# Kernel optimization log

Measured on AMD Instinct MI355X. Metric: run time of the kernel, lower is better.

The kernel has to match this reference:

```python
import jax, jax.numpy as jnp
import numpy as np

B, L, D_MODEL, N_HEADS = 2, 2048, 1024, 16
D_K = D_MODEL // N_HEADS  # 64
THETA = 10000.0


def setup_inputs() -> dict:
    key = jax.random.key(0)
    k1, k2, k3 = jax.random.split(key, 3)
    std_qkv = (2.0 / (D_MODEL + 3 * D_MODEL)) ** 0.5
    std_out = (2.0 / (D_MODEL + D_MODEL)) ** 0.5
    X = jax.random.normal(k1, (B, L, D_MODEL), dtype=jnp.float32)
    Wqkv = jax.random.truncated_normal(k2, -3.0, 3.0, (3 * D_MODEL, D_MODEL), dtype=jnp.float32) * std_qkv
    Wout = jax.random.truncated_normal(k3, -3.0, 3.0, (D_MODEL, D_MODEL), dtype=jnp.float32) * std_out
    token_positions = jnp.arange(B * L, dtype=jnp.int64 if jax.config.jax_enable_x64 else jnp.int32).reshape(B, L)
    return {"X": X, "token_positions": token_positions, "Wqkv": Wqkv, "Wout": Wout}


def _rope(X, pos):
    # X: (b, h, l, d_k); pos: (b, l)
    k = jnp.arange(D_K // 2, dtype=jnp.float32)
    inv_freq = 1.0 / (THETA ** (2.0 * k / D_K))          # (d_k/2,)
    ang = pos[..., None].astype(jnp.float32) * inv_freq  # (b, l, d_k/2)
    cos = jnp.repeat(jnp.cos(ang), 2, axis=-1)[:, None, :, :].astype(X.dtype)  # (b,1,l,d_k)
    sin = jnp.repeat(jnp.sin(ang), 2, axis=-1)[:, None, :, :].astype(X.dtype)
    # interleaved rotation: (x0,x1,x2,x3,...) -> (-x1,x0,-x3,x2,...)
    X_rot = jnp.stack([-X[..., 1::2], X[..., ::2]], axis=-1).reshape(X.shape)
    return X * cos + X_rot * sin


def reference(X, token_positions, Wqkv, Wout):
    b, l, _ = X.shape
    qkv = jnp.einsum('bld,ed->ble', X, Wqkv)  # (b, l, 3*d_model)
    Q, K, V = jnp.split(qkv, 3, axis=-1)
    to_heads = lambda t: t.reshape(b, l, N_HEADS, D_K).transpose(0, 2, 1, 3)  # (b,h,l,dk)
    Q, K, V = to_heads(Q), to_heads(K), to_heads(V)
    Q = _rope(Q, token_positions)
    K = _rope(K, token_positions)
    scores = jnp.einsum('bhqd,bhkd->bhqk', Q, K) / np.float32(np.sqrt(D_K))
    causal = jnp.tril(jnp.ones((l, l), dtype=bool))  # (l, l)
    scores = jnp.where(causal[None, None], scores.astype(jnp.float32), -jnp.inf)
    weights = jax.nn.softmax(scores, axis=-1).astype(X.dtype)
    out = jnp.einsum('bhqk,bhkd->bhqd', weights, V)
    out = out.transpose(0, 2, 1, 3).reshape(b, l, D_MODEL)
    return jnp.einsum('bld,od->blo', out, Wout)
```

## Files before the change

kernel.cpp:

```cpp
#include <hip/hip_runtime.h>
#include <stdint.h>
#include <stddef.h>
#include <math.h>

#define DEVINL __device__ __forceinline__

typedef __attribute__((ext_vector_type(8))) __bf16 bf16x8;
typedef __attribute__((ext_vector_type(4))) float f32x4;
typedef __attribute__((ext_vector_type(4))) unsigned short us4;
typedef __attribute__((ext_vector_type(8))) unsigned short us8;
typedef __attribute__((ext_vector_type(4))) short short4v;

typedef __attribute__((address_space(1))) unsigned int as1_uint;
typedef __attribute__((address_space(3))) unsigned int as3_uint;

constexpr int SEQ    = 2048;
constexpr int DMODEL = 1024;
constexpr int MTOT   = 4096;
constexpr int NQKV   = 3072;
constexpr int DKH    = 64;

constexpr size_t OFF_XBF  = 0;
constexpr size_t OFF_WQKV = OFF_XBF  + (size_t)MTOT * DMODEL * 2;
constexpr size_t OFF_WOUT = OFF_WQKV + (size_t)NQKV * DMODEL * 2;
constexpr size_t OFF_Q    = OFF_WOUT + (size_t)DMODEL * DMODEL * 2;
constexpr size_t OFF_K    = OFF_Q    + (size_t)MTOT * DMODEL * 2;
constexpr size_t OFF_VT   = OFF_K    + (size_t)MTOT * DMODEL * 2;
constexpr size_t OFF_O    = OFF_VT   + (size_t)MTOT * DMODEL * 2;
constexpr size_t OFF_ROPE = OFF_O    + (size_t)MTOT * DMODEL * 2;

constexpr float QSCALE = 0.125f * 1.4426950408889634f;

DEVINL unsigned short f2bf(float f) {
  unsigned int u = __float_as_uint(f);
  u += 0x7fffu + ((u >> 16) & 1u);
  return (unsigned short)(u >> 16);
}

DEVINL float fexp2(float x) { return __builtin_amdgcn_exp2f(x); }

DEVINL void gld_lds16(const unsigned short* g, unsigned short* s) {
  __builtin_amdgcn_global_load_lds((as1_uint*)g, (as3_uint*)s, 16, 0, 0);
}

__global__ __launch_bounds__(256) void prep_kernel(
    const float* __restrict__ X, const float* __restrict__ Wqkv,
    const float* __restrict__ Wout, const int* __restrict__ pos,
    unsigned short* __restrict__ xbf, unsigned short* __restrict__ wqkvbf,
    unsigned short* __restrict__ woutbf, float2* __restrict__ rope) {
  const int t = blockIdx.x * 256 + threadIdx.x;
  if (t < MTOT * 32) {
    const int m = t >> 5, ip = t & 31;
    const float freq = powf(10000.0f, -(float)(2 * ip) / 64.0f);
    const float ang = (float)pos[m] * freq;
    float sv, cv;
    sincosf(ang, &sv, &cv);
    rope[t] = make_float2(cv, sv);
  }
  const int NX = MTOT * DMODEL, NW1 = NQKV * DMODEL, NW2 = DMODEL * DMODEL;
  const int e = t * 4;
  const float* src;
  unsigned short* dst;
  if (e < NX) { src = X + e; dst = xbf + e; }
  else if (e < NX + NW1) { src = Wqkv + (e - NX); dst = wqkvbf + (e - NX); }
  else if (e < NX + NW1 + NW2) { src = Wout + (e - NX - NW1); dst = woutbf + (e - NX - NW1); }
  else return;
  const float4 v = *(const float4*)src;
  us4 o = { f2bf(v.x), f2bf(v.y), f2bf(v.z), f2bf(v.w) };
  *(us4*)dst = o;
}

template <int MODE>
__global__ __launch_bounds__(512) void gemm_kernel(
    const unsigned short* __restrict__ A, const unsigned short* __restrict__ Bw,
    unsigned short* __restrict__ q_out, unsigned short* __restrict__ k_out,
    unsigned short* __restrict__ vt_out, const float2* __restrict__ rope,
    float* __restrict__ f_out) {
  constexpr int K = DMODEL;
  __shared__ __align__(16) unsigned short As[2][2][128 * 32];
  __shared__ __align__(16) unsigned short Bs[2][2][128 * 32];
  const int tid = threadIdx.x;
  const int l = tid & 63, w = tid >> 6;
  const bool producer = (w >= 4);
  const int w4 = w & 3;
  const int g = l >> 4, l15 = l & 15;

  constexpr int GX  = (MODE == 0) ? 24 : 8;
  constexpr int CHN = (MODE == 0) ? 12 : 4;
  const int lid = blockIdx.x + GX * blockIdx.y;
  const int xcd = lid & 7;
  const int sc  = lid >> 3;
  const int bm = (xcd & 3) * 8 + (sc & 7);
  const int bn = (xcd >> 2) * CHN + (sc >> 3);
  const int m0 = bm * 128, n0 = bn * 128;
  const int wm = w4 >> 1, wn = w4 & 1;

  const unsigned short* ag = A  + (size_t)(m0 + w4 * 16 + (l >> 2)) * K + (l & 3) * 8;
  const unsigned short* bg = Bw + (size_t)(n0 + w4 * 16 + (l >> 2)) * K + (l & 3) * 8;

  auto STAGE = [&](int bb, int kt) {
#pragma unroll
    for (int kk = 0; kk < 2; ++kk) {
      const unsigned short* a0 = ag + kt * 64 + kk * 32;
      const unsigned short* b0 = bg + kt * 64 + kk * 32;
      unsigned short* as0 = &As[bb][kk][0] + w4 * 512;
      unsigned short* bs0 = &Bs[bb][kk][0] + w4 * 512;
      gld_lds16(a0, as0);
      gld_lds16(a0 + (size_t)64 * K, as0 + 2048);
      gld_lds16(b0, bs0);
      gld_lds16(b0 + (size_t)64 * K, bs0 + 2048);
    }
  };

  const f32x4 zf = {0.f, 0.f, 0.f, 0.f};
  f32x4 acc[4][4];
#pragma unroll
  for (int i = 0; i < 4; ++i)
#pragma unroll
    for (int j = 0; j < 4; ++j) acc[i][j] = zf;

  if (producer) STAGE(0, 0);
  __syncthreads();
  int cur = 0;

  for (int kt = 0; kt < K / 64; ++kt) {
    if (producer) {
      if (kt + 1 < K / 64) STAGE(cur ^ 1, kt + 1);
    } else {
      bf16x8 af[4][2], bf[4][2];
#pragma unroll
      for (int i = 0; i < 4; ++i)
#pragma unroll
        for (int kk = 0; kk < 2; ++kk) {
          af[i][kk] = *(const bf16x8*)(&As[cur][kk][0] + (wm * 64 + i * 16 + l15) * 32 + g * 8);
          bf[i][kk] = *(const bf16x8*)(&Bs[cur][kk][0] + (wn * 64 + i * 16 + l15) * 32 + g * 8);
        }
#pragma unroll
      for (int i = 0; i < 4; ++i)
#pragma unroll
        for (int j = 0; j < 4; ++j) {
          acc[i][j] = __builtin_amdgcn_mfma_f32_16x16x32_bf16(af[i][0], bf[j][0], acc[i][j], 0, 0, 0);
          acc[i][j] = __builtin_amdgcn_mfma_f32_16x16x32_bf16(af[i][1], bf[j][1], acc[i][j], 0, 0, 0);
        }
    }
    __syncthreads();
    cur ^= 1;
  }

  if (producer) return;

  if constexpr (MODE == 0) {
    const int region = n0 >> 10;
    if (region <= 1) {
      unsigned short* outb = (region == 0) ? q_out : k_out;
      const float qs = (region == 0) ? QSCALE : 1.0f;
#pragma unroll
      for (int i = 0; i < 4; ++i) {
        const int mb = m0 + wm * 64 + i * 16 + g * 4;
#pragma unroll
        for (int j = 0; j < 4; ++j) {
          const int n = n0 + wn * 64 + j * 16 + l15;
          const int ncol = n & 1023;
          const int ip = (n & 63) >> 1;
          const float sgn = (n & 1) ? 1.f : -1.f;
#pragma unroll
          for (int r = 0; r < 4; ++r) {
            const int m = mb + r;
            const float v = acc[i][j][r];
            const float p = __shfl_xor(v, 1);
            const float2 cs = rope[m * 32 + ip];
            const float o = (v * cs.x + sgn * p * cs.y) * qs;
            outb[(size_t)m * DMODEL + ncol] = f2bf(o);
          }
        }
      }
    } else {
#pragma unroll
      for (int i = 0; i < 4; ++i) {
        const int mb = m0 + wm * 64 + i * 16 + g * 4;
        const int b = mb >> 11;
        const int lseq = mb & 2047;
#pragma unroll
        for (int j = 0; j < 4; ++j) {
          const int n = n0 + wn * 64 + j * 16 + l15;
          const int hd = n - 2048;
          us4 o = { f2bf(acc[i][j][0]), f2bf(acc[i][j][1]), f2bf(acc[i][j][2]), f2bf(acc[i][j][3]) };
          *(us4*)(vt_out + (size_t)(b * DMODEL + hd) * SEQ + lseq) = o;
        }
      }
    }
  } else {
#pragma unroll
    for (int i = 0; i < 4; ++i) {
      const int mb = m0 + wm * 64 + i * 16 + g * 4;
#pragma unroll
      for (int j = 0; j < 4; ++j) {
        const int n = n0 + wn * 64 + j * 16 + l15;
#pragma unroll
        for (int r = 0; r < 4; ++r) f_out[(size_t)(mb + r) * DMODEL + n] = acc[i][j][r];
      }
    }
  }
}

__global__ __launch_bounds__(256) void attn_kernel(
    const unsigned short* __restrict__ Qb, const unsigned short* __restrict__ Kb,
    const unsigned short* __restrict__ Vt, unsigned short* __restrict__ Ob) {
  __shared__ __align__(16) unsigned short kv[2][2][4096];
  __shared__ __align__(16) unsigned short Olds[4][16][72];
  const int tid = threadIdx.x;
  const int l = tid & 63, w = tid >> 6;
  const int g = l >> 4, q15 = l & 15;

  const int lid = blockIdx.x + 16 * blockIdx.y;
  const int xcd = lid & 7;
  const int slot = lid >> 3;
  const int bh = xcd * 4 + (slot & 3);
  const int j = slot >> 2;

  const int b = bh >> 4, h = bh & 15;
  const int tA = 31 - j;
  const int tB = j;

  const unsigned short* qpA = Qb + (size_t)(b * SEQ + tA * 64 + w * 16 + q15) * DMODEL + h * DKH + g * 8;
  const unsigned short* qpB = Qb + (size_t)(b * SEQ + tB * 64 + w * 16 + q15) * DMODEL + h * DKH + g * 8;
  const bf16x8 qA0 = *(const bf16x8*)qpA, qA1 = *(const bf16x8*)(qpA + 32);
  const bf16x8 qB0 = *(const bf16x8*)qpB, qB1 = *(const bf16x8*)(qpB + 32);
  const int qselA = tA * 64 + w * 16 + q15;
  const int qselB = tB * 64 + w * 16 + q15;

  const int rS = tid >> 3;
  const int cS = (((tid & 7) * 16) ^ ((rS & 7) << 4)) >> 1;
  const unsigned short* pKg = Kb + (size_t)(b * SEQ + rS) * DMODEL + h * DKH + cS;
  const unsigned short* pVg = Vt + (size_t)(b * DMODEL + h * DKH + rS) * SEQ + cS;

  const int srow = (q15 & 7) << 4;
  const int oc0 = (srow ^ (g * 16)) >> 1;
  const int oc1 = (srow ^ (g * 16 + 64)) >> 1;
  int vc[4];
#pragma unroll
  for (int blk = 0; blk < 4; ++blk) vc[blk] = ((blk * 32 + 8 * g) ^ srow) >> 1;

  const f32x4 zf = {0.f, 0.f, 0.f, 0.f};
  float mrun = -1e30f, lrun = 0.f;
  f32x4 ot[4];
#pragma unroll
  for (int d = 0; d < 4; ++d) ot[d] = zf;

  auto STAGE = [&](int bb, int k0) {
    unsigned short* lk = &kv[bb][0][0] + w * 512;
    unsigned short* lv = &kv[bb][1][0] + w * 512;
    gld_lds16(pKg + (size_t)k0 * DMODEL, lk);
    gld_lds16(pKg + (size_t)(k0 + 32) * DMODEL, lk + 2048);
    gld_lds16(pVg + k0, lv);
    gld_lds16(pVg + (size_t)32 * SEQ + k0, lv + 2048);
  };

  auto STORE = [&](int qt) {
    float lr = lrun;
    lr += __shfl_xor(lr, 16);
    lr += __shfl_xor(lr, 32);
    const float inv = 1.0f / lr;
#pragma unroll
    for (int d = 0; d < 4; ++d) {
      us4 o = { f2bf(ot[d][0] * inv), f2bf(ot[d][1] * inv), f2bf(ot[d][2] * inv), f2bf(ot[d][3] * inv) };
      *(us4*)&Olds[w][q15][d * 16 + g * 4] = o;
    }
    __syncthreads();
    const int r = l >> 2;
    const int c = (l & 3) * 16;
    const us8 v0 = *(const us8*)&Olds[w][r][c];
    const us8 v1 = *(const us8*)&Olds[w][r][c + 8];
    unsigned short* ob = Ob + (size_t)(b * SEQ + qt * 64 + w * 16 + r) * DMODEL + h * DKH + c;
    *(us8*)ob = v0;
    *(us8*)(ob + 8) = v1;
  };

  auto ITER = [&](int cur, int kb0, bf16x8 qf0, bf16x8 qf1, int qsel, bool domask) {
    const unsigned short* lkb = &kv[cur][0][0] + q15 * 64;
    const unsigned short* lvb = &kv[cur][1][0] + q15 * 64;

    float sp[4][4];
    float mt = -1e30f;
#pragma unroll
    for (int blk = 0; blk < 4; ++blk) {
      const bf16x8 kf0 = *(const bf16x8*)(lkb + blk * 1024 + oc0);
      const bf16x8 kf1 = *(const bf16x8*)(lkb + blk * 1024 + oc1);
      f32x4 c = zf;
      c = __builtin_amdgcn_mfma_f32_16x16x32_bf16(kf0, qf0, c, 0, 0, 0);
      c = __builtin_amdgcn_mfma_f32_16x16x32_bf16(kf1, qf1, c, 0, 0, 0);
#pragma unroll
      for (int r = 0; r < 4; ++r) {
        float s = c[r];
        if (domask && (kb0 + blk * 16 + g * 4 + r > qsel)) s = -1e30f;
        sp[blk][r] = s;
        mt = fmaxf(mt, s);
      }
    }
    mt = fmaxf(mt, __shfl_xor(mt, 16));
    mt = fmaxf(mt, __shfl_xor(mt, 32));

    const bool defer = __all(mt - mrun <= 8.0f);
    float mnew, alpha;
    if (defer) { mnew = mrun; alpha = 1.0f; }
    else { mnew = fmaxf(mrun, mt); alpha = fexp2(mrun - mnew); }

    float rs = 0.f;
#pragma unroll
    for (int blk = 0; blk < 4; ++blk)
#pragma unroll
      for (int r = 0; r < 4; ++r) {
        const float p = fexp2(sp[blk][r] - mnew);
        sp[blk][r] = p;
        rs += p;
      }
    if (defer) {
      lrun += rs;
    } else {
      lrun = lrun * alpha + rs;
      mrun = mnew;
#pragma unroll
      for (int d = 0; d < 4; ++d) ot[d] *= alpha;
    }

    short4v pfb[4];
#pragma unroll
    for (int blk = 0; blk < 4; ++blk) {
      union { __bf16 hh[4]; short4v v; } pk;
      pk.hh[0] = (__bf16)sp[blk][0];
      pk.hh[1] = (__bf16)sp[blk][1];
      pk.hh[2] = (__bf16)sp[blk][2];
      pk.hh[3] = (__bf16)sp[blk][3];
      pfb[blk] = pk.v;
    }

    __builtin_amdgcn_s_setprio(1);
#pragma unroll
    for (int dt = 0; dt < 4; ++dt) {
      const unsigned short* vrow = lvb + dt * 1024;
      f32x4 o = ot[dt];
#pragma unroll
      for (int blk = 0; blk < 4; ++blk) {
        const short4v vf = *(const short4v*)(vrow + vc[blk]);
        o = __builtin_amdgcn_mfma_f32_16x16x16bf16_1k(vf, pfb[blk], o, 0, 0, 0);
      }
      ot[dt] = o;
    }
    __builtin_amdgcn_s_setprio(0);
  };

  STAGE(0, 0);
  __syncthreads();
  int cur = 0;

  for (int i = 0; i < tA; ++i) {
    STAGE(cur ^ 1, (i + 1) * 64);
    ITER(cur, i * 64, qA0, qA1, qselA, false);
    __syncthreads();
    cur ^= 1;
  }
  STAGE(cur ^ 1, 0);
  ITER(cur, tA * 64, qA0, qA1, qselA, true);
  STORE(tA);
  mrun = -1e30f; lrun = 0.f;
#pragma unroll
  for (int d = 0; d < 4; ++d) ot[d] = zf;
  __syncthreads();
  cur ^= 1;

  for (int i = 0; i < tB; ++i) {
    STAGE(cur ^ 1, (i + 1) * 64);
    ITER(cur, i * 64, qB0, qB1, qselB, false);
    __syncthreads();
    cur ^= 1;
  }
  ITER(cur, tB * 64, qB0, qB1, qselB, true);
  STORE(tB);
}

extern "C" void kernel_launch(void* const* d_in, const int* in_sizes, int n_in,
                              void* d_out, int out_size, void* d_ws, size_t ws_size,
                              hipStream_t stream) {
  const float* X = (const float*)d_in[0];
  const int* pos = (const int*)d_in[1];
  const float* Wqkv = (const float*)d_in[2];
  const float* Wout = (const float*)d_in[3];
  char* ws = (char*)d_ws;
  unsigned short* xbf    = (unsigned short*)(ws + OFF_XBF);
  unsigned short* wqkvbf = (unsigned short*)(ws + OFF_WQKV);
  unsigned short* woutbf = (unsigned short*)(ws + OFF_WOUT);
  unsigned short* qb     = (unsigned short*)(ws + OFF_Q);
  unsigned short* kbuf   = (unsigned short*)(ws + OFF_K);
  unsigned short* vt     = (unsigned short*)(ws + OFF_VT);
  unsigned short* ob     = (unsigned short*)(ws + OFF_O);
  float2* rope           = (float2*)(ws + OFF_ROPE);

  prep_kernel<<<8192, 256, 0, stream>>>(X, Wqkv, Wout, pos, xbf, wqkvbf, woutbf, rope);
  gemm_kernel<0><<<dim3(NQKV / 128, MTOT / 128), 512, 0, stream>>>(
      xbf, wqkvbf, qb, kbuf, vt, rope, nullptr);
  attn_kernel<<<dim3(16, 32), 256, 0, stream>>>(qb, kbuf, vt, ob);
  gemm_kernel<1><<<dim3(DMODEL / 128, MTOT / 128), 512, 0, stream>>>(
      ob, woutbf, nullptr, nullptr, nullptr, nullptr, (float*)d_out);
}
```

Before: 110.8 us.

## Split attention block into producer and consumer warps for K/V staging

The attention kernel now launches 512 threads per block. Four new producer wavefronts issue the async global-to-LDS K/V loads, and the original four wavefronts only run the MFMA/softmax compute. This is meant to take load-issue instructions off the compute waves. In exchange it doubles the threads per block, which may reduce occupancy, and the barrier per tile still ties producers and consumers together in lockstep.

```diff
diff --git a/kernel.cpp b/kernel.cpp
--- a/kernel.cpp
+++ b/kernel.cpp
@@ -203,14 +203,18 @@
   }
 }
 
-__global__ __launch_bounds__(256) void attn_kernel(
+__global__ __launch_bounds__(512) void attn_kernel(
     const unsigned short* __restrict__ Qb, const unsigned short* __restrict__ Kb,
     const unsigned short* __restrict__ Vt, unsigned short* __restrict__ Ob) {
   __shared__ __align__(16) unsigned short kv[2][2][4096];
   __shared__ __align__(16) unsigned short Olds[4][16][72];
   const int tid = threadIdx.x;
-  const int l = tid & 63, w = tid >> 6;
+  const int l = tid & 63;
+  const int wfull = tid >> 6;
+  const bool producer = (wfull >= 4);
+  const int w = wfull & 3;
   const int g = l >> 4, q15 = l & 15;
+  const int ptid = tid & 255;
 
   const int lid = blockIdx.x + 16 * blockIdx.y;
   const int xcd = lid & 7;
@@ -222,15 +226,18 @@
   const int tA = 31 - j;
   const int tB = j;
 
-  const unsigned short* qpA = Qb + (size_t)(b * SEQ + tA * 64 + w * 16 + q15) * DMODEL + h * DKH + g * 8;
-  const unsigned short* qpB = Qb + (size_t)(b * SEQ + tB * 64 + w * 16 + q15) * DMODEL + h * DKH + g * 8;
-  const bf16x8 qA0 = *(const bf16x8*)qpA, qA1 = *(const bf16x8*)(qpA + 32);
-  const bf16x8 qB0 = *(const bf16x8*)qpB, qB1 = *(const bf16x8*)(qpB + 32);
+  bf16x8 qA0{}, qA1{}, qB0{}, qB1{};
+  if (!producer) {
+    const unsigned short* qpA = Qb + (size_t)(b * SEQ + tA * 64 + w * 16 + q15) * DMODEL + h * DKH + g * 8;
+    const unsigned short* qpB = Qb + (size_t)(b * SEQ + tB * 64 + w * 16 + q15) * DMODEL + h * DKH + g * 8;
+    qA0 = *(const bf16x8*)qpA; qA1 = *(const bf16x8*)(qpA + 32);
+    qB0 = *(const bf16x8*)qpB; qB1 = *(const bf16x8*)(qpB + 32);
+  }
   const int qselA = tA * 64 + w * 16 + q15;
   const int qselB = tB * 64 + w * 16 + q15;
 
-  const int rS = tid >> 3;
-  const int cS = (((tid & 7) * 16) ^ ((rS & 7) << 4)) >> 1;
+  const int rS = ptid >> 3;
+  const int cS = (((ptid & 7) * 16) ^ ((rS & 7) << 4)) >> 1;
   const unsigned short* pKg = Kb + (size_t)(b * SEQ + rS) * DMODEL + h * DKH + cS;
   const unsigned short* pVg = Vt + (size_t)(b * DMODEL + h * DKH + rS) * SEQ + cS;
 
@@ -257,23 +264,27 @@
   };
 
   auto STORE = [&](int qt) {
-    float lr = lrun;
-    lr += __shfl_xor(lr, 16);
-    lr += __shfl_xor(lr, 32);
-    const float inv = 1.0f / lr;
-#pragma unroll
-    for (int d = 0; d < 4; ++d) {
-      us4 o = { f2bf(ot[d][0] * inv), f2bf(ot[d][1] * inv), f2bf(ot[d][2] * inv), f2bf(ot[d][3] * inv) };
-      *(us4*)&Olds[w][q15][d * 16 + g * 4] = o;
+    if (!producer) {
+      float lr = lrun;
+      lr += __shfl_xor(lr, 16);
+      lr += __shfl_xor(lr, 32);
+      const float inv = 1.0f / lr;
+#pragma unroll
+      for (int d = 0; d < 4; ++d) {
+        us4 o = { f2bf(ot[d][0] * inv), f2bf(ot[d][1] * inv), f2bf(ot[d][2] * inv), f2bf(ot[d][3] * inv) };
+        *(us4*)&Olds[w][q15][d * 16 + g * 4] = o;
+      }
     }
     __syncthreads();
-    const int r = l >> 2;
-    const int c = (l & 3) * 16;
-    const us8 v0 = *(const us8*)&Olds[w][r][c];
-    const us8 v1 = *(const us8*)&Olds[w][r][c + 8];
-    unsigned short* ob = Ob + (size_t)(b * SEQ + qt * 64 + w * 16 + r) * DMODEL + h * DKH + c;
-    *(us8*)ob = v0;
-    *(us8*)(ob + 8) = v1;
+    if (!producer) {
+      const int r = l >> 2;
+      const int c = (l & 3) * 16;
+      const us8 v0 = *(const us8*)&Olds[w][r][c];
+      const us8 v1 = *(const us8*)&Olds[w][r][c + 8];
+      unsigned short* ob = Ob + (size_t)(b * SEQ + qt * 64 + w * 16 + r) * DMODEL + h * DKH + c;
+      *(us8*)ob = v0;
+      *(us8*)(ob + 8) = v1;
+    }
   };
 
   auto ITER = [&](int cur, int kb0, bf16x8 qf0, bf16x8 qf1, int qsel, bool domask) {
@@ -349,32 +360,34 @@
     __builtin_amdgcn_s_setprio(0);
   };
 
-  STAGE(0, 0);
+  if (producer) STAGE(0, 0);
   __syncthreads();
   int cur = 0;
 
   for (int i = 0; i < tA; ++i) {
-    STAGE(cur ^ 1, (i + 1) * 64);
-    ITER(cur, i * 64, qA0, qA1, qselA, false);
+    if (producer) STAGE(cur ^ 1, (i + 1) * 64);
+    else ITER(cur, i * 64, qA0, qA1, qselA, false);
     __syncthreads();
     cur ^= 1;
   }
-  STAGE(cur ^ 1, 0);
-  ITER(cur, tA * 64, qA0, qA1, qselA, true);
+  if (producer) STAGE(cur ^ 1, 0);
+  else ITER(cur, tA * 64, qA0, qA1, qselA, true);
   STORE(tA);
-  mrun = -1e30f; lrun = 0.f;
-#pragma unroll
-  for (int d = 0; d < 4; ++d) ot[d] = zf;
+  if (!producer) {
+    mrun = -1e30f; lrun = 0.f;
+#pragma unroll
+    for (int d = 0; d < 4; ++d) ot[d] = zf;
+  }
   __syncthreads();
   cur ^= 1;
 
   for (int i = 0; i < tB; ++i) {
-    STAGE(cur ^ 1, (i + 1) * 64);
-    ITER(cur, i * 64, qB0, qB1, qselB, false);
+    if (producer) STAGE(cur ^ 1, (i + 1) * 64);
+    else ITER(cur, i * 64, qB0, qB1, qselB, false);
     __syncthreads();
     cur ^= 1;
   }
-  ITER(cur, tB * 64, qB0, qB1, qselB, true);
+  if (!producer) ITER(cur, tB * 64, qB0, qB1, qselB, true);
   STORE(tB);
 }
 
@@ -398,7 +411,7 @@
   prep_kernel<<<8192, 256, 0, stream>>>(X, Wqkv, Wout, pos, xbf, wqkvbf, woutbf, rope);
   gemm_kernel<0><<<dim3(NQKV / 128, MTOT / 128), 512, 0, stream>>>(
       xbf, wqkvbf, qb, kbuf, vt, rope, nullptr);
-  attn_kernel<<<dim3(16, 32), 256, 0, stream>>>(qb, kbuf, vt, ob);
+  attn_kernel<<<dim3(16, 32), 512, 0, stream>>>(qb, kbuf, vt, ob);
   gemm_kernel<1><<<dim3(DMODEL / 128, MTOT / 128), 512, 0, stream>>>(
       ob, woutbf, nullptr, nullptr, nullptr, nullptr, (float*)d_out);
 }
```

Result: faster. 105.9 us (median of 2 runs) (-4.5%).
